# Kernel optimization log

Measured on AMD Instinct MI355X. Metric: run time of the kernel, lower is better.

Reference implementation:

```python
import jax, jax.numpy as jnp
import numpy as np

NCLASS = 19


def setup_inputs() -> dict:
    key = jax.random.key(0)
    k1, k2 = jax.random.split(key)
    logits = jax.random.normal(k1, (4, NCLASS, 512, 1024), dtype=jnp.float32)
    target = jax.random.randint(k2, (4, 512, 1024), 0, NCLASS, dtype=jnp.int32)
    return {"logits": logits, "target": target}


def reference(logits, target):
    # Faithful to the torch module: per predicted class cls,
    #   cls_vectors    = logits values at all (c, pixel) positions whose
    #                    argmax-predicted class == cls, grouped per sample n
    #   cls_prototype  = scalar mean of those values per sample
    #   cls_center_loss = mean_n || cls_vectors_n - prototype_n ||_2
    # and the total loss sums over classes. The Python loop + boolean masked
    # select is replaced by one fused segmented reduction using the identity
    #   sum((x - m)^2) = S2 - S1^2 / K   with m = S1/K.
    N, C, H, W = logits.shape
    probs = jax.nn.softmax(logits, axis=1)
    preds = jnp.argmax(probs, axis=1)              # (N, H, W) int

    x = logits.reshape(N, C, H * W)
    s1 = jnp.sum(x, axis=1).reshape(-1)            # (N*HW,) sum over channels per pixel
    s2 = jnp.sum(x * x, axis=1).reshape(-1)        # (N*HW,)
    ones = jnp.ones_like(s1)

    # segment id = sample index * C + predicted class  -> N*C segments
    seg = (preds.reshape(N, -1) + jnp.arange(N, dtype=preds.dtype)[:, None] * C).reshape(-1)
    data = jnp.stack([s1, s2, ones], axis=-1)      # (N*HW, 3)
    sums = jax.ops.segment_sum(data, seg, num_segments=N * C)  # (N*C, 3)
    sums = sums.reshape(N, C, 3)
    S1, S2, cnt = sums[..., 0], sums[..., 1], sums[..., 2]      # (N, nclass)

    # each matching pixel contributes C values => K = cnt * C elements per (n, cls)
    K = jnp.maximum(cnt, 1.0) * C
    sq_dev = jnp.maximum(S2 - S1 * S1 / K, 0.0)    # sum of squared deviations
    norms = jnp.where(cnt > 0, jnp.sqrt(sq_dev), 0.0)           # (N, nclass)

    center_loss = jnp.sum(jnp.mean(norms, axis=0))  # sum over classes of mean over N
    return center_loss
```

## Files before the change

### kernel.cpp

```cpp
#include <hip/hip_runtime.h>

#define NCLS 19
#define NSMP 4
#define HW   (512 * 1024)
#define NSEG (NSMP * NCLS)

__global__ void cl_init_ws(float* ws) {
    int i = threadIdx.x;
    if (i < 3 * NSEG) ws[i] = 0.0f;
}

__global__ __launch_bounds__(256) void cl_main(const float* __restrict__ logits,
                                               float* __restrict__ ws) {
    __shared__ float sS1[NCLS];
    __shared__ float sS2[NCLS];
    __shared__ float sCnt[NCLS];
    const int tid = threadIdx.x;
    if (tid < NCLS) { sS1[tid] = 0.0f; sS2[tid] = 0.0f; sCnt[tid] = 0.0f; }
    __syncthreads();

    const long long p   = ((long long)blockIdx.x * 256 + tid) * 4;
    const int       n   = (int)(p / HW);
    const long long off = p - (long long)n * HW;
    const float* base = logits + (size_t)n * NCLS * HW + off;

    float s1[4], s2[4], mv[4];
    int   mi[4];

    float4 v = *(const float4*)(base);
    {
        const float a0[4] = {v.x, v.y, v.z, v.w};
        #pragma unroll
        for (int j = 0; j < 4; ++j) {
            s1[j] = a0[j];
            s2[j] = a0[j] * a0[j];
            mv[j] = a0[j];
            mi[j] = 0;
        }
    }
    #pragma unroll
    for (int c = 1; c < NCLS; ++c) {
        float4 u = *(const float4*)(base + (size_t)c * HW);
        const float a[4] = {u.x, u.y, u.z, u.w};
        #pragma unroll
        for (int j = 0; j < 4; ++j) {
            s1[j] += a[j];
            s2[j] += a[j] * a[j];
            if (a[j] > mv[j]) { mv[j] = a[j]; mi[j] = c; }
        }
    }

    #pragma unroll
    for (int j = 0; j < 4; ++j) {
        atomicAdd(&sS1[mi[j]],  s1[j]);
        atomicAdd(&sS2[mi[j]],  s2[j]);
        atomicAdd(&sCnt[mi[j]], 1.0f);
    }
    __syncthreads();

    if (tid < NCLS) {
        const int seg = n * NCLS + tid;
        atomicAdd(&ws[seg],            sS1[tid]);
        atomicAdd(&ws[NSEG + seg],     sS2[tid]);
        atomicAdd(&ws[2 * NSEG + seg], sCnt[tid]);
    }
}

__global__ void cl_final(const float* __restrict__ ws, float* __restrict__ out) {
    __shared__ float red[128];
    const int i = threadIdx.x;
    float v = 0.0f;
    if (i < NSEG) {
        const float S1  = ws[i];
        const float S2  = ws[NSEG + i];
        const float cnt = ws[2 * NSEG + i];
        const float K   = fmaxf(cnt, 1.0f) * (float)NCLS;
        const float sq  = fmaxf(S2 - S1 * S1 / K, 0.0f);
        v = (cnt > 0.0f) ? sqrtf(sq) : 0.0f;
    }
    red[i] = v;
    __syncthreads();
    #pragma unroll
    for (int s = 64; s > 0; s >>= 1) {
        if (i < s) red[i] += red[i + s];
        __syncthreads();
    }
    if (i == 0) out[0] = red[0] / (float)NSMP;
}

extern "C" void kernel_launch(void* const* d_in, const int* in_sizes, int n_in,
                              void* d_out, int out_size, void* d_ws, size_t ws_size,
                              hipStream_t stream) {
    const float* logits = (const float*)d_in[0];
    float* ws  = (float*)d_ws;
    float* out = (float*)d_out;

    cl_init_ws<<<1, 256, 0, stream>>>(ws);

    const long long total_pixels = (long long)NSMP * HW;
    const int blocks = (int)(total_pixels / 4 / 256);
    cl_main<<<blocks, 256, 0, stream>>>(logits, ws);

    cl_final<<<1, 128, 0, stream>>>(ws, out);
}
```

Baseline: 58.92 us.

## Process all samples per thread with double-buffered register prefetch

Each thread now handles the same pixel offset across all four samples, cutting the grid from 2048 to 512 blocks. While one sample's 19 float4 channel loads are being reduced, the next sample's loads are issued into a second register buffer. Shared-memory accumulators grow to cover all 76 segments, and the init kernel is replaced by hipMemsetAsync. This raises register pressure substantially (38 float4 live) and lowers occupancy and block count, trading parallelism for memory-level overlap and fewer global atomics per pixel.

```diff
diff --git a/kernel.cpp b/kernel.cpp
--- a/kernel.cpp
+++ b/kernel.cpp
@@ -5,64 +5,65 @@
 #define HW   (512 * 1024)
 #define NSEG (NSMP * NCLS)
 
-__global__ void cl_init_ws(float* ws) {
-    int i = threadIdx.x;
-    if (i < 3 * NSEG) ws[i] = 0.0f;
-}
 
 __global__ __launch_bounds__(256) void cl_main(const float* __restrict__ logits,
                                                float* __restrict__ ws) {
-    __shared__ float sS1[NCLS];
-    __shared__ float sS2[NCLS];
-    __shared__ float sCnt[NCLS];
+    __shared__ float sb[3 * NSEG];
     const int tid = threadIdx.x;
-    if (tid < NCLS) { sS1[tid] = 0.0f; sS2[tid] = 0.0f; sCnt[tid] = 0.0f; }
+    if (tid < 3 * NSEG) sb[tid] = 0.0f;
     __syncthreads();
 
-    const long long p   = ((long long)blockIdx.x * 256 + tid) * 4;
-    const int       n   = (int)(p / HW);
-    const long long off = p - (long long)n * HW;
-    const float* base = logits + (size_t)n * NCLS * HW + off;
+    const size_t off  = (size_t)blockIdx.x * 1024 + (size_t)tid * 4;
+    const float* base = logits + off;
 
-    float s1[4], s2[4], mv[4];
-    int   mi[4];
-
-    float4 v = *(const float4*)(base);
-    {
-        const float a0[4] = {v.x, v.y, v.z, v.w};
-        #pragma unroll
-        for (int j = 0; j < 4; ++j) {
-            s1[j] = a0[j];
-            s2[j] = a0[j] * a0[j];
-            mv[j] = a0[j];
-            mi[j] = 0;
-        }
-    }
-    #pragma unroll
-    for (int c = 1; c < NCLS; ++c) {
-        float4 u = *(const float4*)(base + (size_t)c * HW);
-        const float a[4] = {u.x, u.y, u.z, u.w};
-        #pragma unroll
-        for (int j = 0; j < 4; ++j) {
-            s1[j] += a[j];
-            s2[j] += a[j] * a[j];
-            if (a[j] > mv[j]) { mv[j] = a[j]; mi[j] = c; }
-        }
-    }
+    float4 va[NCLS], vb[NCLS];
 
     #pragma unroll
-    for (int j = 0; j < 4; ++j) {
-        atomicAdd(&sS1[mi[j]],  s1[j]);
-        atomicAdd(&sS2[mi[j]],  s2[j]);
-        atomicAdd(&sCnt[mi[j]], 1.0f);
-    }
+    for (int c = 0; c < NCLS; ++c)
+        va[c] = *(const float4*)(base + (size_t)c * HW);
+
+#define STEP(CUR, NXT, K, DOLOAD)                                              \
+    do {                                                                       \
+        float s1[4], s2[4], mv[4];                                             \
+        int   mi[4];                                                           \
+        _Pragma("unroll")                                                      \
+        for (int c = 0; c < NCLS; ++c) {                                       \
+            if (DOLOAD)                                                        \
+                NXT[c] = *(const float4*)(base + ((size_t)((K) + 1) * NCLS + c) * HW); \
+            const float a[4] = {CUR[c].x, CUR[c].y, CUR[c].z, CUR[c].w};       \
+            _Pragma("unroll")                                                  \
+            for (int j = 0; j < 4; ++j) {                                      \
+                if (c == 0) {                                                  \
+                    s1[j] = a[j]; s2[j] = a[j] * a[j];                         \
+                    mv[j] = a[j]; mi[j] = 0;                                   \
+                } else {                                                       \
+                    s1[j] += a[j];                                             \
+                    s2[j]  = fmaf(a[j], a[j], s2[j]);                          \
+                    if (a[j] > mv[j]) { mv[j] = a[j]; mi[j] = c; }             \
+                }                                                              \
+            }                                                                  \
+        }                                                                      \
+        _Pragma("unroll")                                                      \
+        for (int j = 0; j < 4; ++j) {                                          \
+            atomicAdd(&sb[0 * NSEG + (K) * NCLS + mi[j]], s1[j]);              \
+            atomicAdd(&sb[1 * NSEG + (K) * NCLS + mi[j]], s2[j]);              \
+            atomicAdd(&sb[2 * NSEG + (K) * NCLS + mi[j]], 1.0f);               \
+        }                                                                      \
+                                \
+        asm volatile("" ::: "memory");                                         \
+    } while (0)
+
+    STEP(va, vb, 0, true);
+    STEP(vb, va, 1, true);
+    STEP(va, vb, 2, true);
+    STEP(vb, va, 3, false);
+#undef STEP
+
     __syncthreads();
-
-    if (tid < NCLS) {
-        const int seg = n * NCLS + tid;
-        atomicAdd(&ws[seg],            sS1[tid]);
-        atomicAdd(&ws[NSEG + seg],     sS2[tid]);
-        atomicAdd(&ws[2 * NSEG + seg], sCnt[tid]);
+    if (tid < NSEG) {
+        atomicAdd(&ws[tid],            sb[tid]);
+        atomicAdd(&ws[NSEG + tid],     sb[NSEG + tid]);
+        atomicAdd(&ws[2 * NSEG + tid], sb[2 * NSEG + tid]);
     }
 }
 
@@ -95,11 +96,7 @@
     float* ws  = (float*)d_ws;
     float* out = (float*)d_out;
 
-    cl_init_ws<<<1, 256, 0, stream>>>(ws);
-
-    const long long total_pixels = (long long)NSMP * HW;
-    const int blocks = (int)(total_pixels / 4 / 256);
-    cl_main<<<blocks, 256, 0, stream>>>(logits, ws);
-
+    hipMemsetAsync(ws, 0, 3 * NSEG * sizeof(float), stream);
+    cl_main<<<512, 256, 0, stream>>>(logits, ws);
     cl_final<<<1, 128, 0, stream>>>(ws, out);
 }
```

Result: slower. 61.02 us (+3.6%).
